# Kernel tuning notes

Hardware: AMD Instinct MI355X
Metric: run time of the kernel (lower is better)

Reference implementation:

```python
import jax, jax.numpy as jnp
import numpy as np

N = 100_000   # nodes
E = 1_600_000 # edges
F = 128       # node feature dim
H = 128       # hidden dim
A = 8         # num actions


def setup_inputs() -> dict:
    key = jax.random.key(0)
    ks = jax.random.split(key, 8)
    x = jax.random.normal(ks[0], (N, F), dtype=jnp.float32)
    edge_index = jax.random.randint(ks[1], (2, E), 0, N, dtype=jnp.int64)
    s1 = 1.0 / np.sqrt(F)
    s2 = 1.0 / np.sqrt(H)
    W1 = jax.random.uniform(ks[2], (F, H), jnp.float32, -s1, s1)
    b1 = jnp.zeros((H,), jnp.float32)
    W2 = jax.random.uniform(ks[3], (H, H), jnp.float32, -s2, s2)
    b2 = jnp.zeros((H,), jnp.float32)
    Wfc = jax.random.uniform(ks[4], (H, A), jnp.float32, -s2, s2)
    bfc = jax.random.uniform(ks[5], (A,), jnp.float32, -s2, s2)
    return {"x": x, "edge_index": edge_index, "W1": W1, "b1": b1,
            "W2": W2, "b2": b2, "Wfc": Wfc, "bfc": bfc}


def _gcn_norm(edge_index):
    # PyG GCNConv default: add self-loops, symmetric deg^{-1/2} A deg^{-1/2}
    src, dst = edge_index[0], edge_index[1]
    loop = jnp.arange(N, dtype=src.dtype)
    src_f = jnp.concatenate([src, loop])
    dst_f = jnp.concatenate([dst, loop])
    deg = jax.ops.segment_sum(jnp.ones((E + N,), jnp.float32), dst_f,
                              num_segments=N)
    dis = jax.lax.rsqrt(deg)  # deg >= 1 thanks to self-loops
    norm = dis[src_f] * dis[dst_f]  # [E+N]
    return src_f, dst_f, norm


def _gcn_conv(h, W, b, src_f, dst_f, norm):
    hw = h @ W                              # [N, out]
    msg = hw[src_f] * norm[:, None]         # gather + scale: [E+N, out]
    out = jax.ops.segment_sum(msg, dst_f, num_segments=N)  # scatter-add
    return out + b


def reference(x, edge_index, W1, b1, W2, b2, Wfc, bfc):
    src_f, dst_f, norm = _gcn_norm(edge_index)
    h = jax.nn.relu(_gcn_conv(x, W1, b1, src_f, dst_f, norm))
    h = jax.nn.relu(_gcn_conv(h, W2, b2, src_f, dst_f, norm))
    return h @ Wfc + bfc  # [N, A] per-node Q-values
```

## Files before the change

### kernel.cpp

```cpp
#include <hip/hip_runtime.h>
#include <hip/hip_bf16.h>

#define NN 100000
#define EE 1600000
#define FF 128
#define HH 128
#define AA 8

#define NBIN 782
#define CAP  3072
#define BINBLK 256

typedef unsigned int u32;
typedef unsigned short ushort_t;

using bf16x8 = __attribute__((ext_vector_type(8))) short;
using f32x4  = __attribute__((ext_vector_type(4))) float;

__device__ inline u32 packbf2(float a, float b) {
    __hip_bfloat162 t;
    t.x = __float2bfloat16(a);
    t.y = __float2bfloat16(b);
    return *(u32*)&t;
}
__device__ inline float2 unpackbf2(u32 v) {
    union { u32 u; float f; } lo, hi;
    lo.u = v << 16;
    hi.u = v & 0xffff0000u;
    return make_float2(lo.f, hi.f);
}

__global__ void k_init(int* bincnt) {
    int i = blockIdx.x * blockDim.x + threadIdx.x;
    if (i < NBIN) bincnt[i] = 0;
}

__global__ __launch_bounds__(256)
void k_wt2(const float* __restrict__ W1, const float* __restrict__ W2,
           u32* __restrict__ WT1, u32* __restrict__ WT2) {
    __shared__ float tile[32][33];
    const float* W  = (blockIdx.x < 16) ? W1 : W2;
    u32*         WT = (blockIdx.x < 16) ? WT1 : WT2;
    const int bid = blockIdx.x & 15;
    const int tk = (bid >> 2) * 32;
    const int tn = (bid & 3) * 32;
    const int t = threadIdx.x;
    {
        int r = t >> 3, c4 = t & 7;
        float4 v = *(const float4*)&W[(tk + r) * 128 + tn + c4 * 4];
        tile[r][c4 * 4 + 0] = v.x;
        tile[r][c4 * 4 + 1] = v.y;
        tile[r][c4 * 4 + 2] = v.z;
        tile[r][c4 * 4 + 3] = v.w;
    }
    __syncthreads();
    {
        int nl = t >> 3, w = t & 7;
        u32 w0 = packbf2(tile[w * 4 + 0][nl], tile[w * 4 + 1][nl]);
        u32 w1 = packbf2(tile[w * 4 + 2][nl], tile[w * 4 + 3][nl]);
        *(uint2*)&WT[(size_t)(tn + nl) * 64 + (tk >> 1) + w * 2] = make_uint2(w0, w1);
    }
}

__global__ __launch_bounds__(1024)
void k_bin(const int* __restrict__ ei, int* __restrict__ g_bincnt,
           int2* __restrict__ binbuf, int e) {
    __shared__ int cnt_l[NBIN];
    __shared__ int base_l[NBIN];
    __shared__ int cur_l[NBIN];
    const int t = threadIdx.x;
    for (int q = t; q < NBIN; q += 1024) cnt_l[q] = 0;
    __syncthreads();
    const int per = (((e + BINBLK - 1) / BINBLK) + 3) & ~3;
    const int i0 = blockIdx.x * per;
    const int i1 = min(e, i0 + per);
    int i = i0 + t * 4;
    for (; i + 3 < i1; i += 4096) {
        int4 d4 = *(const int4*)&ei[e + i];
        atomicAdd(&cnt_l[d4.x >> 7], 1);
        atomicAdd(&cnt_l[d4.y >> 7], 1);
        atomicAdd(&cnt_l[d4.z >> 7], 1);
        atomicAdd(&cnt_l[d4.w >> 7], 1);
    }
    for (int j = i; j < min(i + 4, i1); j++)
        atomicAdd(&cnt_l[ei[e + j] >> 7], 1);
    __syncthreads();
    for (int q = t; q < NBIN; q += 1024) {
        base_l[q] = cnt_l[q] ? atomicAdd(&g_bincnt[q], cnt_l[q]) : 0;
        cur_l[q] = 0;
    }
    __syncthreads();
    i = i0 + t * 4;
    for (; i + 3 < i1; i += 4096) {
        int4 s4 = *(const int4*)&ei[i];
        int4 d4 = *(const int4*)&ei[e + i];
        int p0 = d4.x >> 7, p1 = d4.y >> 7, p2 = d4.z >> 7, p3 = d4.w >> 7;
        int q0 = base_l[p0] + atomicAdd(&cur_l[p0], 1);
        int q1 = base_l[p1] + atomicAdd(&cur_l[p1], 1);
        int q2 = base_l[p2] + atomicAdd(&cur_l[p2], 1);
        int q3 = base_l[p3] + atomicAdd(&cur_l[p3], 1);
        if (q0 < CAP) binbuf[(size_t)p0 * CAP + q0] = make_int2(s4.x, d4.x);
        if (q1 < CAP) binbuf[(size_t)p1 * CAP + q1] = make_int2(s4.y, d4.y);
        if (q2 < CAP) binbuf[(size_t)p2 * CAP + q2] = make_int2(s4.z, d4.z);
        if (q3 < CAP) binbuf[(size_t)p3 * CAP + q3] = make_int2(s4.w, d4.w);
    }
    for (int j = i; j < min(i + 4, i1); j++) {
        int dst = ei[e + j], src = ei[j];
        int p = dst >> 7;
        int pos = base_l[p] + atomicAdd(&cur_l[p], 1);
        if (pos < CAP) binbuf[(size_t)p * CAP + pos] = make_int2(src, dst);
    }
}

__global__ __launch_bounds__(1024)
void k_binscan(const int* __restrict__ bincnt, int* __restrict__ binbase) {
    __shared__ int s[1024];
    const int t = threadIdx.x;
    int v = (t < NBIN) ? min(bincnt[t], CAP) : 0;
    s[t] = v;
    __syncthreads();
    for (int off = 1; off < 1024; off <<= 1) {
        int x = (t >= off) ? s[t - off] : 0;
        __syncthreads();
        s[t] += x;
        __syncthreads();
    }
    if (t < NBIN) binbase[t] = s[t] - v;
}

__global__ __launch_bounds__(256)
void k_csr(const int2* __restrict__ binbuf, const int* __restrict__ g_bincnt,
           const int* __restrict__ binbase, int* __restrict__ row_start,
           float* __restrict__ dis, int* __restrict__ csr_src, int n)
{
    __shared__ int deg[128], s[128], cur[128];
    const int p = blockIdx.x;
    const int t = threadIdx.x;
    const int plo = p << 7;
    if (t < 128) { deg[t] = 0; cur[t] = 0; }
    __syncthreads();
    const int c = min(g_bincnt[p], CAP);
    const int2* slab = &binbuf[(size_t)p * CAP];
    for (int i = t; i < c; i += 256)
        atomicAdd(&deg[slab[i].y - plo], 1);
    __syncthreads();
    if (t < 128) s[t] = deg[t];
    __syncthreads();
    for (int off = 1; off < 128; off <<= 1) {
        int x = (t < 128 && t >= off) ? s[t - off] : 0;
        __syncthreads();
        if (t < 128) s[t] += x;
        __syncthreads();
    }
    const int base = binbase[p];
    if (t < 128) {
        int node = plo + t;
        if (node <= n) row_start[node] = base + s[t] - deg[t];
        if (node < n)  dis[node] = rsqrtf((float)deg[t] + 1.0f);
        if (p == NBIN - 1 && t == 127) row_start[n] = base + s[127];
    }
    __syncthreads();
    for (int i = t; i < c; i += 256) {
        int2 sd = slab[i];
        int nl = sd.y - plo;
        int pos = base + (s[nl] - deg[nl]) + atomicAdd(&cur[nl], 1);
        csr_src[pos] = sd.x;
    }
}

#define LDK 136

template<int AF32>
__global__ __launch_bounds__(256)
void k_gemm_mfma(const void* __restrict__ Ain, const u32* __restrict__ WT,
                 const float* __restrict__ dis, u32* __restrict__ outbf, int n)
{
    __shared__ ushort_t sA[64 * LDK];
    __shared__ ushort_t sB[128 * LDK];
    const int tid = threadIdx.x;
    const int row0 = blockIdx.x * 64;

    if (AF32) {
        const float* A = (const float*)Ain;
#pragma unroll
        for (int i = 0; i < 8; i++) {
            int f = tid + i * 256;
            int r = f >> 5, c4 = f & 31;
            int gr = row0 + r; if (gr >= n) gr = n - 1;
            float4 v = *(const float4*)&A[(size_t)gr * 128 + c4 * 4];
            *(uint2*)&sA[r * LDK + c4 * 4] =
                make_uint2(packbf2(v.x, v.y), packbf2(v.z, v.w));
        }
    } else {
        const u32* A = (const u32*)Ain;
#pragma unroll
        for (int i = 0; i < 4; i++) {
            int f = tid + i * 256;
            int r = f >> 4, q = f & 15;
            int gr = row0 + r; if (gr >= n) gr = n - 1;
            uint4 v = *(const uint4*)&A[(size_t)gr * 64 + q * 4];
            *(uint4*)&sA[r * LDK + q * 8] = v;
        }
    }
#pragma unroll
    for (int i = 0; i < 8; i++) {
        int f = tid + i * 256;
        int r = f >> 4, q = f & 15;
        uint4 v = *(const uint4*)&WT[(size_t)r * 64 + q * 4];
        *(uint4*)&sB[r * LDK + q * 8] = v;
    }
    __syncthreads();

    const int l   = tid & 63;
    const int w   = tid >> 6;
    const int col = l & 15;
    const int g   = l >> 4;
    const ushort_t* pa = &sA[(w * 16 + col) * LDK + g * 8];
    const ushort_t* pb = &sB[col * LDK + g * 8];

    f32x4 acc[8] = {};
#pragma unroll
    for (int ks = 0; ks < 4; ks++) {
        bf16x8 a = *(const bf16x8*)(pa + ks * 32);
#pragma unroll
        for (int cf = 0; cf < 8; cf++) {
            bf16x8 b = *(const bf16x8*)(pb + (size_t)cf * 16 * LDK + ks * 32);
            acc[cf] = __builtin_amdgcn_mfma_f32_16x16x32_bf16(a, b, acc[cf], 0, 0, 0);
        }
    }

    const int grow0 = row0 + w * 16 + g * 4;
    float dvr[4];
#pragma unroll
    for (int r = 0; r < 4; r++)
        dvr[r] = (grow0 + r < n) ? dis[grow0 + r] : 0.f;
#pragma unroll
    for (int cf = 0; cf < 8; cf++) {
#pragma unroll
        for (int r = 0; r < 4; r++) {
            float val = acc[cf][r] * dvr[r];
            float oth = __shfl_xor(val, 1);
            if (!(l & 1) && (grow0 + r < n))
                outbf[(size_t)(grow0 + r) * 64 + (cf * 16 + col) / 2] = packbf2(val, oth);
        }
    }
}

__launch_bounds__(256)
__global__ void k_agg(const int* __restrict__ csr_src,
                      const int* __restrict__ row_start,
                      const u32* __restrict__ hw,
                      const float* __restrict__ dis,
                      const float* __restrict__ b,
                      u32* __restrict__ out, int n)
{
    int node = blockIdx.x * 4 + (threadIdx.x >> 6);
    if (node >= n) return;
    int lane = threadIdx.x & 63;
    int beg = row_start[node];
    int end = row_start[node + 1];

    float2 acc = unpackbf2(hw[(long long)node * 64 + lane]);
    int i = beg;
    for (; i + 15 < end; i += 16) {
        int idx[16];
#pragma unroll
        for (int u = 0; u < 16; u++) idx[u] = csr_src[i + u];
        u32 a[16];
#pragma unroll
        for (int u = 0; u < 16; u++) a[u] = hw[(long long)idx[u] * 64 + lane];
        float sx = 0.f, sy = 0.f;
#pragma unroll
        for (int u = 0; u < 16; u++) {
            float2 v = unpackbf2(a[u]);
            sx += v.x; sy += v.y;
        }
        acc.x += sx; acc.y += sy;
    }
    if (i + 7 < end) {
        int idx[8];
#pragma unroll
        for (int u = 0; u < 8; u++) idx[u] = csr_src[i + u];
        u32 a[8];
#pragma unroll
        for (int u = 0; u < 8; u++) a[u] = hw[(long long)idx[u] * 64 + lane];
        float sx = 0.f, sy = 0.f;
#pragma unroll
        for (int u = 0; u < 8; u++) {
            float2 v = unpackbf2(a[u]);
            sx += v.x; sy += v.y;
        }
        acc.x += sx; acc.y += sy;
        i += 8;
    }
    for (; i + 1 < end; i += 2) {
        int s0 = csr_src[i];
        int s1 = csr_src[i + 1];
        float2 v0 = unpackbf2(hw[(long long)s0 * 64 + lane]);
        float2 v1 = unpackbf2(hw[(long long)s1 * 64 + lane]);
        acc.x += v0.x + v1.x;
        acc.y += v0.y + v1.y;
    }
    if (i < end) {
        float2 v0 = unpackbf2(hw[(long long)csr_src[i] * 64 + lane]);
        acc.x += v0.x;
        acc.y += v0.y;
    }
    float d = dis[node];
    float2 bb = *(const float2*)&b[lane * 2];
    float ox = fmaxf(fmaf(d, acc.x, bb.x), 0.f);
    float oy = fmaxf(fmaf(d, acc.y, bb.y), 0.f);
    out[(long long)node * 64 + lane] = packbf2(ox, oy);
}

__launch_bounds__(256)
__global__ void k_fc(const u32* __restrict__ hbf,
                     const float* __restrict__ Wfc,
                     const float* __restrict__ bfc,
                     float* __restrict__ out, int n)
{
    __shared__ float sW[128 * 8];
    __shared__ float sH[32][132];
    const int tid = threadIdx.x;
    *(float4*)&sW[tid * 4] = *(const float4*)&Wfc[tid * 4];
    const int n0 = blockIdx.x * 32;
#pragma unroll
    for (int i = 0; i < 4; i++) {
        int f = tid + i * 256;
        int node = f >> 5;
        int wq = f & 31;
        int gn = n0 + node; if (gn >= n) gn = n - 1;
        uint2 v = *(const uint2*)&hbf[(long long)gn * 64 + wq * 2];
        float2 p0 = unpackbf2(v.x);
        float2 p1 = unpackbf2(v.y);
        sH[node][wq * 4 + 0] = p0.x;
        sH[node][wq * 4 + 1] = p0.y;
        sH[node][wq * 4 + 2] = p1.x;
        sH[node][wq * 4 + 3] = p1.y;
    }
    __syncthreads();
    const int node = tid >> 3;
    const int a = tid & 7;
    float acc = bfc[a];
#pragma unroll
    for (int k = 0; k < 128; k++)
        acc += sH[node][k] * sW[k * 8 + a];
    int gn = n0 + node;
    if (gn < n) out[gn * 8 + a] = acc;
}

extern "C" void kernel_launch(void* const* d_in, const int* in_sizes, int n_in,
                              void* d_out, int out_size, void* d_ws, size_t ws_size,
                              hipStream_t stream) {
    const float* x   = (const float*)d_in[0];
    const int*   ei  = (const int*)d_in[1];
    const float* W1  = (const float*)d_in[2];
    const float* b1  = (const float*)d_in[3];
    const float* W2  = (const float*)d_in[4];
    const float* b2  = (const float*)d_in[5];
    const float* Wfc = (const float*)d_in[6];
    const float* bfc = (const float*)d_in[7];
    float* out = (float*)d_out;

    const int n = NN, e = EE;

    char* ws = (char*)d_ws;
    const size_t MB = 1 << 20;
    float* dis       = (float*)(ws);
    int*   row_start = (int*)  (ws + 512 * 1024);
    int*   bincnt    = (int*)  (ws + 1 * MB);
    int*   binbase   = (int*)  (ws + 1 * MB + 8192);
    u32*   WT1       = (u32*)  (ws + 1 * MB + 65536);
    u32*   WT2       = (u32*)  (ws + 1 * MB + 2 * 65536);
    int2*  binbuf    = (int2*) (ws + 2 * MB);
    int*   csr_src   = (int*)  (ws + 22 * MB);
    u32*   hwbf      = (u32*)  (ws + 29 * MB);
    u32*   hbf       = (u32*)  (ws + 55 * MB);

    k_init<<<(NBIN + 255) / 256, 256, 0, stream>>>(bincnt);
    k_wt2<<<32, 256, 0, stream>>>(W1, W2, WT1, WT2);

    k_bin<<<BINBLK, 1024, 0, stream>>>(ei, bincnt, binbuf, e);
    k_binscan<<<1, 1024, 0, stream>>>(bincnt, binbase);
    k_csr<<<NBIN, 256, 0, stream>>>(binbuf, bincnt, binbase, row_start, dis, csr_src, n);

    const int gemm_grid = (n + 63) / 64;
    const int agg_grid  = (n + 3) / 4;

    k_gemm_mfma<1><<<gemm_grid, 256, 0, stream>>>(x, WT1, dis, hwbf, n);
    k_agg<<<agg_grid, 256, 0, stream>>>(csr_src, row_start, hwbf, dis, b1, hbf, n);

    k_gemm_mfma<0><<<gemm_grid, 256, 0, stream>>>(hbf, WT2, dis, hwbf, n);
    k_agg<<<agg_grid, 256, 0, stream>>>(csr_src, row_start, hwbf, dis, b2, hbf, n);

    k_fc<<<(n + 31) / 32, 256, 0, stream>>>(hbf, Wfc, bfc, out, n);
}
```

Before: 217.6 us.

## Fuse final FC into second aggregation and fold bin scan into CSR build

The final linear layer now runs inside the second aggregation kernel: each wavefront computes partial dot products against Wfc and reduces them with cross-lane shuffles, so the bf16 hidden state is never written and re-read. The standalone bin-prefix-scan kernel is removed; each CSR block instead sums the counts of all earlier bins itself, and the init kernel is replaced by a memset. This cuts two launches and one global round trip, at the cost of 48 shuffles per node in the fused kernel and redundant prefix sums across CSR blocks.

```diff
diff --git a/kernel.cpp b/kernel.cpp
--- a/kernel.cpp
+++ b/kernel.cpp
@@ -28,11 +28,6 @@
     lo.u = v << 16;
     hi.u = v & 0xffff0000u;
     return make_float2(lo.f, hi.f);
-}
-
-__global__ void k_init(int* bincnt) {
-    int i = blockIdx.x * blockDim.x + threadIdx.x;
-    if (i < NBIN) bincnt[i] = 0;
 }
 
 __global__ __launch_bounds__(256)
@@ -112,33 +107,29 @@
     }
 }
 
-__global__ __launch_bounds__(1024)
-void k_binscan(const int* __restrict__ bincnt, int* __restrict__ binbase) {
-    __shared__ int s[1024];
-    const int t = threadIdx.x;
-    int v = (t < NBIN) ? min(bincnt[t], CAP) : 0;
-    s[t] = v;
-    __syncthreads();
-    for (int off = 1; off < 1024; off <<= 1) {
-        int x = (t >= off) ? s[t - off] : 0;
-        __syncthreads();
-        s[t] += x;
-        __syncthreads();
-    }
-    if (t < NBIN) binbase[t] = s[t] - v;
-}
-
 __global__ __launch_bounds__(256)
 void k_csr(const int2* __restrict__ binbuf, const int* __restrict__ g_bincnt,
-           const int* __restrict__ binbase, int* __restrict__ row_start,
-           float* __restrict__ dis, int* __restrict__ csr_src, int n)
+           int* __restrict__ row_start, float* __restrict__ dis,
+           int* __restrict__ csr_src, int n)
 {
     __shared__ int deg[128], s[128], cur[128];
+    __shared__ int red[256];
     const int p = blockIdx.x;
     const int t = threadIdx.x;
     const int plo = p << 7;
+
+    int psum = 0;
+    for (int q = t; q < p; q += 256) psum += min(g_bincnt[q], CAP);
+    red[t] = psum;
     if (t < 128) { deg[t] = 0; cur[t] = 0; }
     __syncthreads();
+#pragma unroll
+    for (int off = 128; off > 0; off >>= 1) {
+        if (t < off) red[t] += red[t + off];
+        __syncthreads();
+    }
+    const int base = red[0];
+
     const int c = min(g_bincnt[p], CAP);
     const int2* slab = &binbuf[(size_t)p * CAP];
     for (int i = t; i < c; i += 256)
@@ -152,7 +143,6 @@
         if (t < 128) s[t] += x;
         __syncthreads();
     }
-    const int base = binbase[p];
     if (t < 128) {
         int node = plo + t;
         if (node <= n) row_start[node] = base + s[t] - deg[t];
@@ -246,13 +236,17 @@
     }
 }
 
+template<int FC>
 __launch_bounds__(256)
 __global__ void k_agg(const int* __restrict__ csr_src,
                       const int* __restrict__ row_start,
                       const u32* __restrict__ hw,
                       const float* __restrict__ dis,
                       const float* __restrict__ b,
-                      u32* __restrict__ out, int n)
+                      u32* __restrict__ outbf,
+                      const float* __restrict__ Wfc,
+                      const float* __restrict__ bfc,
+                      float* __restrict__ outfc, int n)
 {
     int node = blockIdx.x * 4 + (threadIdx.x >> 6);
     if (node >= n) return;
@@ -310,43 +304,32 @@
     float2 bb = *(const float2*)&b[lane * 2];
     float ox = fmaxf(fmaf(d, acc.x, bb.x), 0.f);
     float oy = fmaxf(fmaf(d, acc.y, bb.y), 0.f);
-    out[(long long)node * 64 + lane] = packbf2(ox, oy);
-}
-
-__launch_bounds__(256)
-__global__ void k_fc(const u32* __restrict__ hbf,
-                     const float* __restrict__ Wfc,
-                     const float* __restrict__ bfc,
-                     float* __restrict__ out, int n)
-{
-    __shared__ float sW[128 * 8];
-    __shared__ float sH[32][132];
-    const int tid = threadIdx.x;
-    *(float4*)&sW[tid * 4] = *(const float4*)&Wfc[tid * 4];
-    const int n0 = blockIdx.x * 32;
-#pragma unroll
-    for (int i = 0; i < 4; i++) {
-        int f = tid + i * 256;
-        int node = f >> 5;
-        int wq = f & 31;
-        int gn = n0 + node; if (gn >= n) gn = n - 1;
-        uint2 v = *(const uint2*)&hbf[(long long)gn * 64 + wq * 2];
-        float2 p0 = unpackbf2(v.x);
-        float2 p1 = unpackbf2(v.y);
-        sH[node][wq * 4 + 0] = p0.x;
-        sH[node][wq * 4 + 1] = p0.y;
-        sH[node][wq * 4 + 2] = p1.x;
-        sH[node][wq * 4 + 3] = p1.y;
-    }
-    __syncthreads();
-    const int node = tid >> 3;
-    const int a = tid & 7;
-    float acc = bfc[a];
-#pragma unroll
-    for (int k = 0; k < 128; k++)
-        acc += sH[node][k] * sW[k * 8 + a];
-    int gn = n0 + node;
-    if (gn < n) out[gn * 8 + a] = acc;
+
+    if (!FC) {
+        outbf[(long long)node * 64 + lane] = packbf2(ox, oy);
+    } else {
+        const float4 w0a = *(const float4*)&Wfc[(lane * 2) * 8];
+        const float4 w0b = *(const float4*)&Wfc[(lane * 2) * 8 + 4];
+        const float4 w1a = *(const float4*)&Wfc[(lane * 2 + 1) * 8];
+        const float4 w1b = *(const float4*)&Wfc[(lane * 2 + 1) * 8 + 4];
+        float p[8];
+        p[0] = ox * w0a.x + oy * w1a.x;
+        p[1] = ox * w0a.y + oy * w1a.y;
+        p[2] = ox * w0a.z + oy * w1a.z;
+        p[3] = ox * w0a.w + oy * w1a.w;
+        p[4] = ox * w0b.x + oy * w1b.x;
+        p[5] = ox * w0b.y + oy * w1b.y;
+        p[6] = ox * w0b.z + oy * w1b.z;
+        p[7] = ox * w0b.w + oy * w1b.w;
+#pragma unroll
+        for (int off = 1; off < 64; off <<= 1) {
+#pragma unroll
+            for (int a = 0; a < 8; a++)
+                p[a] += __shfl_xor(p[a], off);
+        }
+        if (lane < 8)
+            outfc[(size_t)node * 8 + lane] = p[lane] + bfc[lane];
+    }
 }
 
 extern "C" void kernel_launch(void* const* d_in, const int* in_sizes, int n_in,
@@ -369,7 +352,6 @@
     float* dis       = (float*)(ws);
     int*   row_start = (int*)  (ws + 512 * 1024);
     int*   bincnt    = (int*)  (ws + 1 * MB);
-    int*   binbase   = (int*)  (ws + 1 * MB + 8192);
     u32*   WT1       = (u32*)  (ws + 1 * MB + 65536);
     u32*   WT2       = (u32*)  (ws + 1 * MB + 2 * 65536);
     int2*  binbuf    = (int2*) (ws + 2 * MB);
@@ -377,21 +359,20 @@
     u32*   hwbf      = (u32*)  (ws + 29 * MB);
     u32*   hbf       = (u32*)  (ws + 55 * MB);
 
-    k_init<<<(NBIN + 255) / 256, 256, 0, stream>>>(bincnt);
+    hipMemsetAsync(bincnt, 0, NBIN * sizeof(int), stream);
     k_wt2<<<32, 256, 0, stream>>>(W1, W2, WT1, WT2);
 
     k_bin<<<BINBLK, 1024, 0, stream>>>(ei, bincnt, binbuf, e);
-    k_binscan<<<1, 1024, 0, stream>>>(bincnt, binbase);
-    k_csr<<<NBIN, 256, 0, stream>>>(binbuf, bincnt, binbase, row_start, dis, csr_src, n);
+    k_csr<<<NBIN, 256, 0, stream>>>(binbuf, bincnt, row_start, dis, csr_src, n);
 
     const int gemm_grid = (n + 63) / 64;
     const int agg_grid  = (n + 3) / 4;
 
     k_gemm_mfma<1><<<gemm_grid, 256, 0, stream>>>(x, WT1, dis, hwbf, n);
-    k_agg<<<agg_grid, 256, 0, stream>>>(csr_src, row_start, hwbf, dis, b1, hbf, n);
+    k_agg<0><<<agg_grid, 256, 0, stream>>>(csr_src, row_start, hwbf, dis, b1,
+                                           hbf, nullptr, nullptr, nullptr, n);
 
     k_gemm_mfma<0><<<gemm_grid, 256, 0, stream>>>(hbf, WT2, dis, hwbf, n);
-    k_agg<<<agg_grid, 256, 0, stream>>>(csr_src, row_start, hwbf, dis, b2, hbf, n);
-
-    k_fc<<<(n + 31) / 32, 256, 0, stream>>>(hbf, Wfc, bfc, out, n);
-}
+    k_agg<1><<<agg_grid, 256, 0, stream>>>(csr_src, row_start, hwbf, dis, b2,
+                                           nullptr, Wfc, bfc, out, n);
+}
```

Result: no change. 215.3 us (-1.0%).
